# Optimization experiments

Hardware: AMD Instinct MI355X
Metric: run time of the kernel (lower is better)

Reference implementation:

```python
import jax, jax.numpy as jnp
import numpy as np


def setup_inputs() -> dict:
    key = jax.random.key(0)
    k1, k2 = jax.random.split(key)
    n = 16384
    y = jax.random.normal(k1, (n,), dtype=jnp.float32)          # sign = event indicator, |y| = time
    y_hat = jax.random.normal(k2, (n, 1), dtype=jnp.float32)    # risk scores
    return {"y": y, "y_hat": y_hat}


def reference(y, y_hat):
    T = jnp.abs(y)                       # [n] observed times
    E = (y > 0).astype(jnp.float32)      # [n] event indicator (1 = uncensored)
    theta = y_hat.reshape(-1)            # [n]
    # Risk set: R[i, j] = 1 if T[j] >= T[i]
    R = (T[None, :] >= T[:, None]).astype(theta.dtype)  # [n, n]
    risk_sum = jnp.sum(jnp.exp(theta)[None, :] * R, axis=1)     # [n]
    loss = -jnp.mean((theta - jnp.log(risk_sum)) * E)
    return loss
```

## Files before the change

### kernel.cpp

```cpp
#include <hip/hip_runtime.h>


constexpr int   B     = 4096;
constexpr int   C     = 64;
constexpr float SCALE = 512.0f;

__global__ __launch_bounds__(256) void k_zero(int* zbase, int nwords)
{
    const int i = blockIdx.x * 256 + threadIdx.x;
    if (i < nwords) zbase[i] = 0;
}

__global__ __launch_bounds__(256) void k_fill(
    const float* __restrict__ y, const float* __restrict__ yhat,
    int* __restrict__ cnt, float* __restrict__ bw, float2* __restrict__ padded)
{
    const int i = blockIdx.x * 256 + threadIdx.x;
    const float T = fabsf(y[i]);
    const float w = expf(yhat[i]);
    int b = (int)(T * SCALE);
    b = (b > B - 1) ? (B - 1) : b;
    atomicAdd(&bw[b], w);
    const int pos = atomicAdd(&cnt[b], 1);
    if (pos < C) padded[b * C + pos] = make_float2(T, w);
}

__global__ __launch_bounds__(1024) void k_suff(
    const float* __restrict__ bw, float* __restrict__ suff)
{
    __shared__ float wsumF[16];
    __shared__ float woffF[16];

    const int t = threadIdx.x, lane = t & 63, wid = t >> 6;

    float f0 = bw[B - 1 - (t * 4 + 0)], f1 = bw[B - 1 - (t * 4 + 1)];
    float f2 = bw[B - 1 - (t * 4 + 2)], f3 = bw[B - 1 - (t * 4 + 3)];
    const float fsum = f0 + f1 + f2 + f3;
    float xf = fsum;
    for (int off = 1; off < 64; off <<= 1) {
        float v = __shfl_up(xf, off, 64);
        if (lane >= off) xf += v;
    }
    if (lane == 63) wsumF[wid] = xf;
    __syncthreads();
    if (t == 0) {
        float rf = 0.0f;
        for (int w0 = 0; w0 < 16; ++w0) { woffF[w0] = rf; rf += wsumF[w0]; }
    }
    __syncthreads();

    float exf = woffF[wid] + (xf - fsum);
    suff[B - 1 - (t * 4 + 0)] = exf; exf += f0;
    suff[B - 1 - (t * 4 + 1)] = exf; exf += f1;
    suff[B - 1 - (t * 4 + 2)] = exf; exf += f2;
    suff[B - 1 - (t * 4 + 3)] = exf;
}

__global__ __launch_bounds__(256) void k_main(
    const float* __restrict__ y, const float* __restrict__ yhat,
    const int* __restrict__ cnt, const float* __restrict__ suff,
    const float2* __restrict__ padded, float* __restrict__ acc,
    int* __restrict__ done, float* __restrict__ out, int n)
{
    const int i = blockIdx.x * 256 + threadIdx.x;

    const float yi = y[i];
    const float T  = fabsf(yi);
    int b = (int)(T * SCALE);
    b = (b > B - 1) ? (B - 1) : b;

    float rs = suff[b];
    int c = cnt[b];
    c = (c > C) ? C : c;
    const float2* base = padded + (size_t)b * C;
    for (int j = 0; j < c; ++j) {
        const float2 o = base[j];
        rs += (o.x >= T) ? o.y : 0.0f;
    }

    float p = (yi > 0.0f) ? (yhat[i] - logf(rs)) : 0.0f;

#pragma unroll
    for (int off = 32; off > 0; off >>= 1)
        p += __shfl_down(p, off, 64);

    __shared__ float sred[4];
    const int wid = threadIdx.x >> 6, lane = threadIdx.x & 63;
    if (lane == 0) sred[wid] = p;
    __syncthreads();
    if (threadIdx.x == 0) {
        const float bs = sred[0] + sred[1] + sred[2] + sred[3];
        atomicAdd(acc, bs);
        __threadfence();
        const int old = atomicAdd(done, 1);
        if (old == (int)gridDim.x - 1) {
            const float tot = atomicAdd(acc, 0.0f);
            out[0] = -tot / (float)n;
        }
    }
}

extern "C" void kernel_launch(void* const* d_in, const int* in_sizes, int n_in,
                              void* d_out, int out_size, void* d_ws, size_t ws_size,
                              hipStream_t stream) {
    const float* y    = (const float*)d_in[0];
    const float* yhat = (const float*)d_in[1];
    float* out        = (float*)d_out;
    const int n       = in_sizes[0];

    char* p = (char*)d_ws;
    int*    cnt    = (int*)p;      p += (size_t)B * sizeof(int);
    float*  bw     = (float*)p;    p += (size_t)B * sizeof(float);
    float*  acc    = (float*)p;    p += sizeof(float);
    int*    done   = (int*)p;      p += sizeof(int);
    float*  suff   = (float*)p;    p += (size_t)B * sizeof(float);
    float2* padded = (float2*)p;

    const int zwords = 2 * B + 2;
    k_zero<<<dim3((zwords + 255) / 256), dim3(256), 0, stream>>>((int*)d_ws, zwords);
    k_fill<<<dim3(n / 256), dim3(256), 0, stream>>>(y, yhat, cnt, bw, padded);
    k_suff<<<dim3(1), dim3(1024), 0, stream>>>(bw, suff);
    k_main<<<dim3(n / 256), dim3(256), 0, stream>>>(y, yhat, cnt, suff, padded,
                                                    acc, done, out, n);
}
```

Measured before the change: 28.55 us.

## Fuse fill, suffix-scan and main passes into one persistent kernel with grid barriers

Replaces three separate kernel launches (fill, single-block suffix scan, main) with one 64-block persistent kernel that uses atomic grid-wide barriers between phases. The suffix scan is distributed: each block sums the bins above its 64-bin chunk and scans its own chunk. The final reduction writes per-block partial sums and block 0 combines them, replacing the atomic accumulator. This is meant to remove launch gaps and the serial single-block scan. In exchange it depends on all 64 blocks being co-resident and pays spin-wait barrier latency.

```diff
diff --git a/kernel.cpp b/kernel.cpp
--- a/kernel.cpp
+++ b/kernel.cpp
@@ -4,6 +4,7 @@
 constexpr int   B     = 4096;
 constexpr int   C     = 64;
 constexpr float SCALE = 512.0f;
+constexpr int   GRID  = 64;
 
 __global__ __launch_bounds__(256) void k_zero(int* zbase, int nwords)
 {
@@ -11,92 +12,95 @@
     if (i < nwords) zbase[i] = 0;
 }
 
-__global__ __launch_bounds__(256) void k_fill(
+__device__ __forceinline__ void gbar(int* bar, int target)
+{
+    __syncthreads();
+    if (threadIdx.x == 0) {
+        __threadfence();
+        __hip_atomic_fetch_add(bar, 1, __ATOMIC_ACQ_REL, __HIP_MEMORY_SCOPE_AGENT);
+        while (__hip_atomic_load(bar, __ATOMIC_ACQUIRE, __HIP_MEMORY_SCOPE_AGENT) < target) {
+            __builtin_amdgcn_s_sleep(1);
+        }
+        __threadfence();
+    }
+    __syncthreads();
+}
+
+__global__ __launch_bounds__(256) void k_fused(
     const float* __restrict__ y, const float* __restrict__ yhat,
-    int* __restrict__ cnt, float* __restrict__ bw, float2* __restrict__ padded)
+    int* __restrict__ cnt, float* __restrict__ bw, float* __restrict__ suff,
+    float2* __restrict__ padded, float* __restrict__ bsum,
+    int* __restrict__ bar, float* __restrict__ out, int n)
 {
-    const int i = blockIdx.x * 256 + threadIdx.x;
-    const float T = fabsf(y[i]);
-    const float w = expf(yhat[i]);
+    const int bk  = blockIdx.x;
+    const int tid = threadIdx.x;
+    const int i   = bk * 256 + tid;
+    const int lane = tid & 63, wid = tid >> 6;
+
+    __shared__ float sred[4];
+
+    const float yi    = y[i];
+    const float theta = yhat[i];
+    const float T     = fabsf(yi);
+    const float w     = expf(theta);
     int b = (int)(T * SCALE);
     b = (b > B - 1) ? (B - 1) : b;
+
     atomicAdd(&bw[b], w);
     const int pos = atomicAdd(&cnt[b], 1);
     if (pos < C) padded[b * C + pos] = make_float2(T, w);
-}
 
-__global__ __launch_bounds__(1024) void k_suff(
-    const float* __restrict__ bw, float* __restrict__ suff)
-{
-    __shared__ float wsumF[16];
-    __shared__ float woffF[16];
+    gbar(bar, 1 * GRID);
 
-    const int t = threadIdx.x, lane = t & 63, wid = t >> 6;
+    {
+        float part = 0.0f;
+        for (int j = (bk + 1) * 64 + tid; j < B; j += 256) part += bw[j];
+#pragma unroll
+        for (int off = 32; off > 0; off >>= 1) part += __shfl_down(part, off, 64);
+        if (lane == 0) sred[wid] = part;
+        __syncthreads();
+        const float suffOff = sred[0] + sred[1] + sred[2] + sred[3];
 
-    float f0 = bw[B - 1 - (t * 4 + 0)], f1 = bw[B - 1 - (t * 4 + 1)];
-    float f2 = bw[B - 1 - (t * 4 + 2)], f3 = bw[B - 1 - (t * 4 + 3)];
-    const float fsum = f0 + f1 + f2 + f3;
-    float xf = fsum;
-    for (int off = 1; off < 64; off <<= 1) {
-        float v = __shfl_up(xf, off, 64);
-        if (lane >= off) xf += v;
-    }
-    if (lane == 63) wsumF[wid] = xf;
-    __syncthreads();
-    if (t == 0) {
-        float rf = 0.0f;
-        for (int w0 = 0; w0 < 16; ++w0) { woffF[w0] = rf; rf += wsumF[w0]; }
-    }
-    __syncthreads();
-
-    float exf = woffF[wid] + (xf - fsum);
-    suff[B - 1 - (t * 4 + 0)] = exf; exf += f0;
-    suff[B - 1 - (t * 4 + 1)] = exf; exf += f1;
-    suff[B - 1 - (t * 4 + 2)] = exf; exf += f2;
-    suff[B - 1 - (t * 4 + 3)] = exf;
-}
-
-__global__ __launch_bounds__(256) void k_main(
-    const float* __restrict__ y, const float* __restrict__ yhat,
-    const int* __restrict__ cnt, const float* __restrict__ suff,
-    const float2* __restrict__ padded, float* __restrict__ acc,
-    int* __restrict__ done, float* __restrict__ out, int n)
-{
-    const int i = blockIdx.x * 256 + threadIdx.x;
-
-    const float yi = y[i];
-    const float T  = fabsf(yi);
-    int b = (int)(T * SCALE);
-    b = (b > B - 1) ? (B - 1) : b;
-
-    float rs = suff[b];
-    int c = cnt[b];
-    c = (c > C) ? C : c;
-    const float2* base = padded + (size_t)b * C;
-    for (int j = 0; j < c; ++j) {
-        const float2 o = base[j];
-        rs += (o.x >= T) ? o.y : 0.0f;
+        if (wid == 0) {
+            const float v = bw[bk * 64 + lane];
+            float x = v;
+#pragma unroll
+            for (int off = 1; off < 64; off <<= 1) {
+                const float t = __shfl_down(x, off, 64);
+                if (lane + off < 64) x += t;
+            }
+            suff[bk * 64 + lane] = suffOff + x - v;
+        }
     }
 
-    float p = (yi > 0.0f) ? (yhat[i] - logf(rs)) : 0.0f;
+    gbar(bar, 2 * GRID);
 
+    {
+        float rs = suff[b];
+        int c = cnt[b];
+        c = (c > C) ? C : c;
+        const float2* base = padded + (size_t)b * C;
+        for (int j = 0; j < c; ++j) {
+            const float2 o = base[j];
+            rs += (o.x >= T) ? o.y : 0.0f;
+        }
+
+        float p = (yi > 0.0f) ? (theta - logf(rs)) : 0.0f;
 #pragma unroll
-    for (int off = 32; off > 0; off >>= 1)
-        p += __shfl_down(p, off, 64);
+        for (int off = 32; off > 0; off >>= 1) p += __shfl_down(p, off, 64);
+        __syncthreads();
+        if (lane == 0) sred[wid] = p;
+        __syncthreads();
+        if (tid == 0) bsum[bk] = sred[0] + sred[1] + sred[2] + sred[3];
+    }
 
-    __shared__ float sred[4];
-    const int wid = threadIdx.x >> 6, lane = threadIdx.x & 63;
-    if (lane == 0) sred[wid] = p;
-    __syncthreads();
-    if (threadIdx.x == 0) {
-        const float bs = sred[0] + sred[1] + sred[2] + sred[3];
-        atomicAdd(acc, bs);
-        __threadfence();
-        const int old = atomicAdd(done, 1);
-        if (old == (int)gridDim.x - 1) {
-            const float tot = atomicAdd(acc, 0.0f);
-            out[0] = -tot / (float)n;
-        }
+    gbar(bar, 3 * GRID);
+
+    if (bk == 0 && wid == 0) {
+        float v = bsum[lane];
+#pragma unroll
+        for (int off = 32; off > 0; off >>= 1) v += __shfl_down(v, off, 64);
+        if (lane == 0) out[0] = -v / (float)n;
     }
 }
 
@@ -111,15 +115,13 @@
     char* p = (char*)d_ws;
     int*    cnt    = (int*)p;      p += (size_t)B * sizeof(int);
     float*  bw     = (float*)p;    p += (size_t)B * sizeof(float);
-    float*  acc    = (float*)p;    p += sizeof(float);
-    int*    done   = (int*)p;      p += sizeof(int);
+    int*    bar    = (int*)p;      p += sizeof(int);
     float*  suff   = (float*)p;    p += (size_t)B * sizeof(float);
+    float*  bsum   = (float*)p;    p += (size_t)GRID * sizeof(float);
     float2* padded = (float2*)p;
 
-    const int zwords = 2 * B + 2;
+    const int zwords = 2 * B + 1;
     k_zero<<<dim3((zwords + 255) / 256), dim3(256), 0, stream>>>((int*)d_ws, zwords);
-    k_fill<<<dim3(n / 256), dim3(256), 0, stream>>>(y, yhat, cnt, bw, padded);
-    k_suff<<<dim3(1), dim3(1024), 0, stream>>>(bw, suff);
-    k_main<<<dim3(n / 256), dim3(256), 0, stream>>>(y, yhat, cnt, suff, padded,
-                                                    acc, done, out, n);
+    k_fused<<<dim3(GRID), dim3(256), 0, stream>>>(y, yhat, cnt, bw, suff, padded,
+                                                  bsum, bar, out, n);
 }
```

Measured after the change: 42.38 us. +48.4%, slower.

## Fuse suffix-sum scan into main kernel using per-block shared memory

Applied to the files above, without the earlier changes.

Removes the single-block suffix-scan kernel and has each main-kernel block load the bin weights into shared memory and compute the exclusive suffix sum itself. This eliminates one kernel launch and its serialization gap, plus the global round trip of the suffix array. In exchange every block redundantly reads the bin array and scans it, and uses 16KB of LDS per block.

```diff
diff --git a/kernel.cpp b/kernel.cpp
--- a/kernel.cpp
+++ b/kernel.cpp
@@ -4,6 +4,7 @@
 constexpr int   B     = 4096;
 constexpr int   C     = 64;
 constexpr float SCALE = 512.0f;
+constexpr int   BPT   = B / 256;
 
 __global__ __launch_bounds__(256) void k_zero(int* zbase, int nwords)
 {
@@ -25,51 +26,55 @@
     if (pos < C) padded[b * C + pos] = make_float2(T, w);
 }
 
-__global__ __launch_bounds__(1024) void k_suff(
-    const float* __restrict__ bw, float* __restrict__ suff)
+__global__ __launch_bounds__(256) void k_main(
+    const float* __restrict__ y, const float* __restrict__ yhat,
+    const int* __restrict__ cnt, const float* __restrict__ bw,
+    const float2* __restrict__ padded, float* __restrict__ acc,
+    int* __restrict__ done, float* __restrict__ out, int n)
 {
-    __shared__ float wsumF[16];
-    __shared__ float woffF[16];
+    __shared__ float sbw[B];
+    __shared__ float sred[4];
 
-    const int t = threadIdx.x, lane = t & 63, wid = t >> 6;
+    const int tid = threadIdx.x;
+    const int i   = blockIdx.x * 256 + tid;
+    const int lane = tid & 63, wid = tid >> 6;
 
-    float f0 = bw[B - 1 - (t * 4 + 0)], f1 = bw[B - 1 - (t * 4 + 1)];
-    float f2 = bw[B - 1 - (t * 4 + 2)], f3 = bw[B - 1 - (t * 4 + 3)];
-    const float fsum = f0 + f1 + f2 + f3;
-    float xf = fsum;
+    for (int j = tid; j < B; j += 256) sbw[j] = bw[j];
+
+    const float yi    = y[i];
+    const float theta = yhat[i];
+    const float T     = fabsf(yi);
+    int b = (int)(T * SCALE);
+    b = (b > B - 1) ? (B - 1) : b;
+    __syncthreads();
+
+    const int c0 = tid * BPT;
+    float s = 0.0f;
+#pragma unroll
+    for (int k = 0; k < BPT; ++k) s += sbw[c0 + k];
+
+    float x = s;
+#pragma unroll
     for (int off = 1; off < 64; off <<= 1) {
-        float v = __shfl_up(xf, off, 64);
-        if (lane >= off) xf += v;
+        const float t = __shfl_down(x, off, 64);
+        if (lane + off < 64) x += t;
     }
-    if (lane == 63) wsumF[wid] = xf;
+    if (lane == 0) sred[wid] = x;
     __syncthreads();
-    if (t == 0) {
-        float rf = 0.0f;
-        for (int w0 = 0; w0 < 16; ++w0) { woffF[w0] = rf; rf += wsumF[w0]; }
+    float above = 0.0f;
+    for (int w2 = wid + 1; w2 < 4; ++w2) above += sred[w2];
+    __syncthreads();
+
+    float run = above + (x - s);
+#pragma unroll
+    for (int k = BPT - 1; k >= 0; --k) {
+        const float v = sbw[c0 + k];
+        sbw[c0 + k] = run;
+        run += v;
     }
     __syncthreads();
 
-    float exf = woffF[wid] + (xf - fsum);
-    suff[B - 1 - (t * 4 + 0)] = exf; exf += f0;
-    suff[B - 1 - (t * 4 + 1)] = exf; exf += f1;
-    suff[B - 1 - (t * 4 + 2)] = exf; exf += f2;
-    suff[B - 1 - (t * 4 + 3)] = exf;
-}
-
-__global__ __launch_bounds__(256) void k_main(
-    const float* __restrict__ y, const float* __restrict__ yhat,
-    const int* __restrict__ cnt, const float* __restrict__ suff,
-    const float2* __restrict__ padded, float* __restrict__ acc,
-    int* __restrict__ done, float* __restrict__ out, int n)
-{
-    const int i = blockIdx.x * 256 + threadIdx.x;
-
-    const float yi = y[i];
-    const float T  = fabsf(yi);
-    int b = (int)(T * SCALE);
-    b = (b > B - 1) ? (B - 1) : b;
-
-    float rs = suff[b];
+    float rs = sbw[b];
     int c = cnt[b];
     c = (c > C) ? C : c;
     const float2* base = padded + (size_t)b * C;
@@ -78,17 +83,12 @@
         rs += (o.x >= T) ? o.y : 0.0f;
     }
 
-    float p = (yi > 0.0f) ? (yhat[i] - logf(rs)) : 0.0f;
-
+    float p = (yi > 0.0f) ? (theta - logf(rs)) : 0.0f;
 #pragma unroll
-    for (int off = 32; off > 0; off >>= 1)
-        p += __shfl_down(p, off, 64);
-
-    __shared__ float sred[4];
-    const int wid = threadIdx.x >> 6, lane = threadIdx.x & 63;
+    for (int off = 32; off > 0; off >>= 1) p += __shfl_down(p, off, 64);
     if (lane == 0) sred[wid] = p;
     __syncthreads();
-    if (threadIdx.x == 0) {
+    if (tid == 0) {
         const float bs = sred[0] + sred[1] + sred[2] + sred[3];
         atomicAdd(acc, bs);
         __threadfence();
@@ -113,13 +113,11 @@
     float*  bw     = (float*)p;    p += (size_t)B * sizeof(float);
     float*  acc    = (float*)p;    p += sizeof(float);
     int*    done   = (int*)p;      p += sizeof(int);
-    float*  suff   = (float*)p;    p += (size_t)B * sizeof(float);
     float2* padded = (float2*)p;
 
     const int zwords = 2 * B + 2;
     k_zero<<<dim3((zwords + 255) / 256), dim3(256), 0, stream>>>((int*)d_ws, zwords);
     k_fill<<<dim3(n / 256), dim3(256), 0, stream>>>(y, yhat, cnt, bw, padded);
-    k_suff<<<dim3(1), dim3(1024), 0, stream>>>(bw, suff);
-    k_main<<<dim3(n / 256), dim3(256), 0, stream>>>(y, yhat, cnt, suff, padded,
+    k_main<<<dim3(n / 256), dim3(256), 0, stream>>>(y, yhat, cnt, bw, padded,
                                                     acc, done, out, n);
 }
```

After: 28.10 us. About the same (-1.6%).
